# Optimization experiments

Hardware: AMD Instinct MI355X
Metric: run time of the kernel (lower is better)

## Reference

```python
import jax, jax.numpy as jnp
import numpy as np

N_NODES = 100000
N_EDGES = 1600000
D_IN = 128
D_H = 128
NEG_SLOPE = 0.2  # DGL GATConv default


def gat_layer(x, W, attn_l, attn_r, bias, src, dst, n_nodes):
    # x: [N, Din] -> h: [N, H]  (num_heads=1, head dim squeezed)
    h = x @ W
    el = jnp.einsum('nh,h->n', h, attn_l)  # [N]
    er = jnp.einsum('nh,h->n', h, attn_r)  # [N]
    e = jax.nn.leaky_relu(el[src] + er[dst], NEG_SLOPE)  # [E]
    # edge softmax over incoming edges of each dst node (numerically stable)
    m = jax.ops.segment_max(e, dst, num_segments=n_nodes)  # [N], -inf on zero-in-degree
    ex = jnp.exp(e - m[dst])  # [E]
    s = jax.ops.segment_sum(ex, dst, num_segments=n_nodes)  # [N]
    a = ex / s[dst]  # [E]
    out = jax.ops.segment_sum(a[:, None] * h[src], dst, num_segments=n_nodes)  # [N, H]
    return out + bias


def setup_inputs() -> dict:
    key = jax.random.key(0)
    ks = jax.random.split(key, 16)
    feat = jax.random.normal(ks[0], (N_NODES, D_IN), dtype=jnp.float32)
    src = jax.random.randint(ks[1], (N_EDGES,), 0, N_NODES, dtype=jnp.int32)
    dst = jax.random.randint(ks[2], (N_EDGES,), 0, N_NODES, dtype=jnp.int32)
    def xavier(k, shape):
        fan = sum(shape)
        return jax.random.normal(k, shape, dtype=jnp.float32) * jnp.sqrt(2.0 / fan)
    params = {}
    dims = [D_IN, D_H, D_H]
    for i in range(3):
        params[f'W{i+1}'] = xavier(ks[3 + 4 * i], (dims[i], D_H))
        params[f'al{i+1}'] = xavier(ks[4 + 4 * i], (D_H,))
        params[f'ar{i+1}'] = xavier(ks[5 + 4 * i], (D_H,))
        params[f'b{i+1}'] = jnp.zeros((D_H,), dtype=jnp.float32)
    return dict(feat=feat, src=src, dst=dst, **params)


def reference(feat, src, dst, W1, al1, ar1, b1, W2, al2, ar2, b2, W3, al3, ar3, b3):
    n = feat.shape[0]
    h = gat_layer(feat, W1, al1, ar1, b1, src, dst, n)
    h = gat_layer(h, W2, al2, ar2, b2, src, dst, n)
    h = gat_layer(h, W3, al3, ar3, b3, src, dst, n)
    return h  # [N, H] (head dim of size 1 squeezed)
```

## Files before the change

### kernel.cpp

```cpp
#include <hip/hip_runtime.h>

#define DH 128
#define NBMAX 1024
#define BCH 8192

typedef __attribute__((ext_vector_type(8))) short s16x8;
typedef __attribute__((ext_vector_type(4))) float f32x4;

__device__ __forceinline__ ushort f2bf(float x) {
  uint u = __builtin_bit_cast(uint, x);
  u = (u + 0x7FFF + ((u >> 16) & 1)) >> 16;
  return (ushort)u;
}
__device__ __forceinline__ float bfl2f(uint u) {
  return __builtin_bit_cast(float, u << 16);
}
__device__ __forceinline__ float bfh2f(uint u) {
  return __builtin_bit_cast(float, u & 0xFFFF0000u);
}


__global__ __launch_bounds__(256) void chist_kernel(const int* __restrict__ dst,
                                                    int* __restrict__ chist, int E, int NB) {
  __shared__ int h[NBMAX];
  int t = threadIdx.x;
  for (int i = t; i < NB; i += 256) h[i] = 0;
  __syncthreads();
  int base = blockIdx.x * BCH;
  int n = min(BCH, E - base);
  for (int i = t; i < n; i += 256) atomicAdd(&h[((uint)dst[base + i]) >> 7], 1);
  __syncthreads();
  for (int i = t; i < NB; i += 256)
    if (h[i]) atomicAdd(&chist[i * 16], h[i]);
}

__global__ __launch_bounds__(256) void cscan_kernel(const int* __restrict__ chist,
                                                    int* __restrict__ cbase, int* __restrict__ ccur,
                                                    int* __restrict__ rowptr, int N, int NB, int E) {
  __shared__ int lds[256];
  int t = threadIdx.x;
  int v[4], s = 0;
#pragma unroll
  for (int j = 0; j < 4; ++j) {
    int idx = t * 4 + j;
    v[j] = (idx < NB) ? chist[idx * 16] : 0;
    s += v[j];
  }
  lds[t] = s;
  __syncthreads();
  for (int off = 1; off < 256; off <<= 1) {
    int add = (t >= off) ? lds[t - off] : 0;
    __syncthreads();
    lds[t] += add;
    __syncthreads();
  }
  int run = t ? lds[t - 1] : 0;
#pragma unroll
  for (int j = 0; j < 4; ++j) {
    int idx = t * 4 + j;
    if (idx < NB) {
      cbase[idx] = run;
      ccur[idx * 16] = run;
    }
    run += v[j];
  }
  if (t == 255) cbase[NB] = lds[255];
  if (t == 0) rowptr[N] = E;
}

__global__ __launch_bounds__(256) void binscat_kernel(const int* __restrict__ src,
                                                      const int* __restrict__ dst,
                                                      int* __restrict__ ccur,
                                                      uint2* __restrict__ puv, int E, int NB) {
  __shared__ int h[NBMAX];
  __shared__ int gb[NBMAX];
  int t = threadIdx.x;
  int base = blockIdx.x * BCH;
  int n = min(BCH, E - base);
  for (int i = t; i < NB; i += 256) h[i] = 0;
  __syncthreads();
  for (int i = t; i < n; i += 256) atomicAdd(&h[((uint)dst[base + i]) >> 7], 1);
  __syncthreads();
  for (int i = t; i < NB; i += 256) {
    int c = h[i];
    gb[i] = c ? atomicAdd(&ccur[i * 16], c) : 0;
    h[i] = 0;
  }
  __syncthreads();
  for (int i = t; i < n; i += 256) {
    int d = dst[base + i];
    int b = ((uint)d) >> 7;
    int p = gb[b] + atomicAdd(&h[b], 1);
    puv[p] = make_uint2((uint)src[base + i], (uint)d);
  }
}

__global__ __launch_bounds__(256) void finesort_kernel(const uint2* __restrict__ puv,
                                                       const int* __restrict__ cbase,
                                                       int* __restrict__ rowptr,
                                                       int* __restrict__ ssrc, int N) {
  int b = blockIdx.x;
  int base = cbase[b];
  int cnt = cbase[b + 1] - base;
  __shared__ int ncnt[128], nincl[128], noff[128];
  int t = threadIdx.x;
  if (t < 128) ncnt[t] = 0;
  __syncthreads();
  for (int i = t; i < cnt; i += 256) atomicAdd(&ncnt[puv[base + i].y & 127], 1);
  __syncthreads();
  if (t < 128) nincl[t] = ncnt[t];
  __syncthreads();
  for (int off = 1; off < 128; off <<= 1) {
    int add = (t < 128 && t >= off) ? nincl[t - off] : 0;
    __syncthreads();
    if (t < 128) nincl[t] += add;
    __syncthreads();
  }
  if (t < 128) {
    noff[t] = nincl[t] - ncnt[t];
    int node = (b << 7) + t;
    if (node < N) rowptr[node] = base + noff[t];
    ncnt[t] = 0;
  }
  __syncthreads();
  for (int i = t; i < cnt; i += 256) {
    uint2 e = puv[base + i];
    int ln = e.y & 127;
    int p = base + noff[ln] + atomicAdd(&ncnt[ln], 1);
    ssrc[p] = (int)e.x;
  }
}

__global__ __launch_bounds__(256) void wt_kernel(const float* __restrict__ W,
                                                 ushort* __restrict__ Wtb) {
  int i = blockIdx.x * 256 + threadIdx.x;
  int col = i >> 7, k = i & 127;
  Wtb[(size_t)col * DH + k] = f2bf(W[(size_t)k * DH + col]);
}

template <bool XF32>
__global__ __launch_bounds__(256) void gemm_kernel(const void* __restrict__ xin,
                                                   const ushort* __restrict__ Wtb,
                                                   const float* __restrict__ al,
                                                   const float* __restrict__ ar,
                                                   ushort* __restrict__ hb,
                                                   float* __restrict__ el,
                                                   float* __restrict__ er, int M) {
  __shared__ ushort As[64 * DH];
  __shared__ ushort Bs[DH * DH];
  int t = threadIdx.x;
  int R0 = blockIdx.x * 64;

  for (int i = t; i < 2048; i += 256) {
    int col = i >> 4, kb = i & 15;
    s16x8 v = *(const s16x8*)(Wtb + (size_t)col * DH + kb * 8);
    *(s16x8*)(&Bs[col * DH + ((kb ^ (col & 15)) * 8)]) = v;
  }
  for (int i = t; i < 1024; i += 256) {
    int row = i >> 4, kb = i & 15;
    int gr = R0 + row;
    s16x8 v;
    if (gr < M) {
      if constexpr (XF32) {
        const float4* p = (const float4*)((const float*)xin + (size_t)gr * DH + kb * 8);
        float4 a = p[0], b = p[1];
        v[0] = (short)f2bf(a.x); v[1] = (short)f2bf(a.y);
        v[2] = (short)f2bf(a.z); v[3] = (short)f2bf(a.w);
        v[4] = (short)f2bf(b.x); v[5] = (short)f2bf(b.y);
        v[6] = (short)f2bf(b.z); v[7] = (short)f2bf(b.w);
      } else {
        v = *(const s16x8*)((const ushort*)xin + (size_t)gr * DH + kb * 8);
      }
    } else {
      v = (s16x8)0;
    }
    *(s16x8*)(&As[row * DH + ((kb ^ (row & 15)) * 8)]) = v;
  }
  __syncthreads();

  int w = t >> 6, lane = t & 63;
  int li = lane & 15, lq = lane >> 4;
  f32x4 acc[8] = {};
  int arow = w * 16 + li;
#pragma unroll
  for (int kc = 0; kc < 4; ++kc) {
    int kb = kc * 4 + lq;
    s16x8 af = *(const s16x8*)(&As[arow * DH + ((kb ^ (arow & 15)) * 8)]);
#pragma unroll
    for (int cf = 0; cf < 8; ++cf) {
      int bcol = cf * 16 + li;
      s16x8 bf = *(const s16x8*)(&Bs[bcol * DH + ((kb ^ (bcol & 15)) * 8)]);
      acc[cf] = __builtin_amdgcn_mfma_f32_16x16x32_bf16(af, bf, acc[cf], 0, 0, 0);
    }
  }

  int Rw = R0 + w * 16;
  float alv[8], arv[8];
#pragma unroll
  for (int cf = 0; cf < 8; ++cf) {
    alv[cf] = al[cf * 16 + li];
    arv[cf] = ar[cf * 16 + li];
  }
#pragma unroll
  for (int r = 0; r < 4; ++r) {
    float sl = 0.f, sr = 0.f;
#pragma unroll
    for (int cf = 0; cf < 8; ++cf) {
      sl += acc[cf][r] * alv[cf];
      sr += acc[cf][r] * arv[cf];
    }
#pragma unroll
    for (int off = 1; off <= 8; off <<= 1) {
      sl += __shfl_xor(sl, off);
      sr += __shfl_xor(sr, off);
    }
    int grow = Rw + lq * 4 + r;
    if (li == 0 && grow < M) {
      el[grow] = sl;
      er[grow] = sr;
    }
  }

  ushort* hl = &As[w * 16 * DH];
#pragma unroll
  for (int cf = 0; cf < 8; ++cf)
#pragma unroll
    for (int r = 0; r < 4; ++r) hl[(lq * 4 + r) * DH + cf * 16 + li] = f2bf(acc[cf][r]);
  __syncthreads();
#pragma unroll
  for (int p = 0; p < 4; ++p) {
    int row = lane >> 2;
    int blk = (lane & 3) + p * 4;
    s16x8 v = *(const s16x8*)(&hl[row * DH + blk * 8]);
    int grow = Rw + row;
    if (grow < M) *(s16x8*)(hb + (size_t)grow * DH + blk * 8) = v;
  }
}

template <int FINAL>
__global__ __launch_bounds__(256) void agg_kernel(const ushort* __restrict__ hb,
                                                  const float* __restrict__ el,
                                                  const float* __restrict__ er,
                                                  const int* __restrict__ rowptr,
                                                  const int* __restrict__ ssrc,
                                                  const float* __restrict__ bias,
                                                  void* __restrict__ outv, int M) {
  int wid = (blockIdx.x * blockDim.x + threadIdx.x) >> 6;
  int lane = threadIdx.x & 63;
  if (wid >= M) return;
  int begin = rowptr[wid], end = rowptr[wid + 1];
  float2 b2 = ((const float2*)bias)[lane];
  int deg = end - begin;
  float acc0 = 0.f, acc1 = 0.f;
  float inv = 0.f;

  if (deg > 0 && deg <= 64) {
    int e = begin + lane;
    int idx = (e < end) ? ssrc[e] : 0;
    float sc = -1e30f;
    if (e < end) {
      sc = el[idx] + er[wid];
      sc = sc > 0.f ? sc : 0.2f * sc;
    }
    float mx = sc;
#pragma unroll
    for (int off = 32; off; off >>= 1) mx = fmaxf(mx, __shfl_xor(mx, off));
    float wgt = (e < end) ? __expf(sc - mx) : 0.f;
    float ssum = wgt;
#pragma unroll
    for (int off = 32; off; off >>= 1) ssum += __shfl_xor(ssum, off);

    int j = 0;
    for (; j + 16 <= deg; j += 16) {
      uint u[16];
      float wg[16];
#pragma unroll
      for (int k = 0; k < 16; ++k) {
        int s = __shfl(idx, j + k);
        wg[k] = __shfl(wgt, j + k);
        u[k] = ((const uint*)(hb + (size_t)s * DH))[lane];
      }
#pragma unroll
      for (int k = 0; k < 16; ++k) {
        acc0 += wg[k] * bfl2f(u[k]);
        acc1 += wg[k] * bfh2f(u[k]);
      }
    }
    for (; j + 4 <= deg; j += 4) {
      uint u[4];
      float wg[4];
#pragma unroll
      for (int k = 0; k < 4; ++k) {
        int s = __shfl(idx, j + k);
        wg[k] = __shfl(wgt, j + k);
        u[k] = ((const uint*)(hb + (size_t)s * DH))[lane];
      }
#pragma unroll
      for (int k = 0; k < 4; ++k) {
        acc0 += wg[k] * bfl2f(u[k]);
        acc1 += wg[k] * bfh2f(u[k]);
      }
    }
    for (; j < deg; ++j) {
      int s = __shfl(idx, j);
      float wg = __shfl(wgt, j);
      uint u = ((const uint*)(hb + (size_t)s * DH))[lane];
      acc0 += wg * bfl2f(u);
      acc1 += wg * bfh2f(u);
    }
    inv = 1.f / ssum;
  } else if (deg > 64) {
    float er_d = er[wid];
    float mx = -1e30f;
    for (int e = begin + lane; e < end; e += 64) {
      float s = el[ssrc[e]] + er_d;
      s = s > 0.f ? s : 0.2f * s;
      mx = fmaxf(mx, s);
    }
#pragma unroll
    for (int off = 32; off; off >>= 1) mx = fmaxf(mx, __shfl_xor(mx, off));
    float ssum_l = 0.f;
    for (int base = begin; base < end; base += 64) {
      int n = min(64, end - base);
      int e = base + lane;
      int idx = 0;
      float wgt = 0.f;
      if (lane < n) {
        idx = ssrc[e];
        float sc = el[idx] + er_d;
        sc = sc > 0.f ? sc : 0.2f * sc;
        wgt = __expf(sc - mx);
      }
      ssum_l += wgt;
      int j = 0;
      for (; j + 4 <= n; j += 4) {
        uint u[4];
        float wg[4];
#pragma unroll
        for (int k = 0; k < 4; ++k) {
          int s = __shfl(idx, j + k);
          wg[k] = __shfl(wgt, j + k);
          u[k] = ((const uint*)(hb + (size_t)s * DH))[lane];
        }
#pragma unroll
        for (int k = 0; k < 4; ++k) {
          acc0 += wg[k] * bfl2f(u[k]);
          acc1 += wg[k] * bfh2f(u[k]);
        }
      }
      for (; j < n; ++j) {
        int s = __shfl(idx, j);
        float wg = __shfl(wgt, j);
        uint u = ((const uint*)(hb + (size_t)s * DH))[lane];
        acc0 += wg * bfl2f(u);
        acc1 += wg * bfh2f(u);
      }
    }
#pragma unroll
    for (int off = 32; off; off >>= 1) ssum_l += __shfl_xor(ssum_l, off);
    inv = 1.f / ssum_l;
  }
  float o0 = acc0 * inv + b2.x;
  float o1 = acc1 * inv + b2.y;
  if constexpr (FINAL) {
    ((float2*)((float*)outv + (size_t)wid * DH))[lane] = make_float2(o0, o1);
  } else {
    uint p = (uint)f2bf(o0) | ((uint)f2bf(o1) << 16);
    ((uint*)((ushort*)outv + (size_t)wid * DH))[lane] = p;
  }
}

extern "C" void kernel_launch(void* const* d_in, const int* in_sizes, int n_in,
                              void* d_out, int out_size, void* d_ws, size_t ws_size,
                              hipStream_t stream) {
  const float* feat = (const float*)d_in[0];
  const int* src = (const int*)d_in[1];
  const int* dst = (const int*)d_in[2];
  const int N = in_sizes[0] / DH;
  const int E = in_sizes[1];
  const int NB = (N + 127) >> 7;
  const float* W[3]  = {(const float*)d_in[3], (const float*)d_in[7],  (const float*)d_in[11]};
  const float* al[3] = {(const float*)d_in[4], (const float*)d_in[8],  (const float*)d_in[12]};
  const float* ar[3] = {(const float*)d_in[5], (const float*)d_in[9],  (const float*)d_in[13]};
  const float* bi[3] = {(const float*)d_in[6], (const float*)d_in[10], (const float*)d_in[14]};

  char* ws = (char*)d_ws;
  size_t off = 0;
  auto alloc = [&](size_t bytes) {
    void* p = ws + off;
    off = (off + bytes + 255) & ~(size_t)255;
    return p;
  };
  ushort* hb   = (ushort*)alloc((size_t)N * DH * sizeof(ushort));
  ushort* xb   = (ushort*)alloc((size_t)N * DH * sizeof(ushort));
  float* el    = (float*)alloc((size_t)N * sizeof(float));
  float* er    = (float*)alloc((size_t)N * sizeof(float));
  int* rowptr  = (int*)alloc((size_t)(N + 1) * sizeof(int));
  int* ssrc    = (int*)alloc((size_t)E * sizeof(int));
  ushort* Wtb  = (ushort*)alloc((size_t)DH * DH * sizeof(ushort));
  int* chist   = (int*)alloc((size_t)NBMAX * 16 * sizeof(int));
  int* cbase   = (int*)alloc((size_t)(NBMAX + 1) * sizeof(int));
  int* ccur    = (int*)alloc((size_t)NBMAX * 16 * sizeof(int));
  uint2* puv   = (uint2*)hb;

  hipMemsetAsync(chist, 0, (size_t)NBMAX * 16 * sizeof(int), stream);
  int ebl = (E + BCH - 1) / BCH;
  chist_kernel<<<ebl, 256, 0, stream>>>(dst, chist, E, NB);
  cscan_kernel<<<1, 256, 0, stream>>>(chist, cbase, ccur, rowptr, N, NB, E);
  binscat_kernel<<<ebl, 256, 0, stream>>>(src, dst, ccur, puv, E, NB);
  finesort_kernel<<<NB, 256, 0, stream>>>(puv, cbase, rowptr, ssrc, N);

  for (int l = 0; l < 3; ++l) {
    wt_kernel<<<64, 256, 0, stream>>>(W[l], Wtb);
    if (l == 0)
      gemm_kernel<true><<<(N + 63) / 64, 256, 0, stream>>>(feat, Wtb, al[l], ar[l], hb, el, er, N);
    else
      gemm_kernel<false><<<(N + 63) / 64, 256, 0, stream>>>(xb, Wtb, al[l], ar[l], hb, el, er, N);
    if (l < 2)
      agg_kernel<0><<<(N + 3) / 4, 256, 0, stream>>>(hb, el, er, rowptr, ssrc, bi[l], xb, N);
    else
      agg_kernel<1><<<(N + 3) / 4, 256, 0, stream>>>(hb, el, er, rowptr, ssrc, bi[l], d_out, N);
  }
}
```

Before: 344.8 us.

## Pack sort keys into 32 bits and gather 16-byte rows per quarter-wave in aggregation

The bin scatter now stores each edge as one 32-bit word, with the low 7 bits of dst in the top bits and src in the low 25 bits, instead of a uint2. This halves the scatter and fine-sort traffic. In the low-degree aggregation path, each quarter-wave now loads a full 256-byte row as 16-byte vectors, so four edges are gathered per instruction. Partial sums are then reduced across quarters with shuffles and written by 16 lanes using vector stores. The change adds cross-lane reduction cost and assumes node ids fit in 25 bits, and it drops the unrolling in the high-degree path.

```diff
diff --git a/kernel.cpp b/kernel.cpp
--- a/kernel.cpp
+++ b/kernel.cpp
@@ -71,7 +71,7 @@
 __global__ __launch_bounds__(256) void binscat_kernel(const int* __restrict__ src,
                                                       const int* __restrict__ dst,
                                                       int* __restrict__ ccur,
-                                                      uint2* __restrict__ puv, int E, int NB) {
+                                                      uint* __restrict__ puv, int E, int NB) {
   __shared__ int h[NBMAX];
   __shared__ int gb[NBMAX];
   int t = threadIdx.x;
@@ -88,14 +88,14 @@
   }
   __syncthreads();
   for (int i = t; i < n; i += 256) {
-    int d = dst[base + i];
-    int b = ((uint)d) >> 7;
+    uint d = (uint)dst[base + i];
+    int b = d >> 7;
     int p = gb[b] + atomicAdd(&h[b], 1);
-    puv[p] = make_uint2((uint)src[base + i], (uint)d);
-  }
-}
-
-__global__ __launch_bounds__(256) void finesort_kernel(const uint2* __restrict__ puv,
+    puv[p] = ((d & 127u) << 25) | (uint)src[base + i];
+  }
+}
+
+__global__ __launch_bounds__(256) void finesort_kernel(const uint* __restrict__ puv,
                                                        const int* __restrict__ cbase,
                                                        int* __restrict__ rowptr,
                                                        int* __restrict__ ssrc, int N) {
@@ -106,7 +106,7 @@
   int t = threadIdx.x;
   if (t < 128) ncnt[t] = 0;
   __syncthreads();
-  for (int i = t; i < cnt; i += 256) atomicAdd(&ncnt[puv[base + i].y & 127], 1);
+  for (int i = t; i < cnt; i += 256) atomicAdd(&ncnt[puv[base + i] >> 25], 1);
   __syncthreads();
   if (t < 128) nincl[t] = ncnt[t];
   __syncthreads();
@@ -124,10 +124,10 @@
   }
   __syncthreads();
   for (int i = t; i < cnt; i += 256) {
-    uint2 e = puv[base + i];
-    int ln = e.y & 127;
+    uint e = puv[base + i];
+    int ln = e >> 25;
     int p = base + noff[ln] + atomicAdd(&ncnt[ln], 1);
-    ssrc[p] = (int)e.x;
+    ssrc[p] = (int)(e & 0x1FFFFFFu);
   }
 }
 
@@ -249,67 +249,9 @@
   int lane = threadIdx.x & 63;
   if (wid >= M) return;
   int begin = rowptr[wid], end = rowptr[wid + 1];
-  float2 b2 = ((const float2*)bias)[lane];
   int deg = end - begin;
-  float acc0 = 0.f, acc1 = 0.f;
-  float inv = 0.f;
-
-  if (deg > 0 && deg <= 64) {
-    int e = begin + lane;
-    int idx = (e < end) ? ssrc[e] : 0;
-    float sc = -1e30f;
-    if (e < end) {
-      sc = el[idx] + er[wid];
-      sc = sc > 0.f ? sc : 0.2f * sc;
-    }
-    float mx = sc;
-#pragma unroll
-    for (int off = 32; off; off >>= 1) mx = fmaxf(mx, __shfl_xor(mx, off));
-    float wgt = (e < end) ? __expf(sc - mx) : 0.f;
-    float ssum = wgt;
-#pragma unroll
-    for (int off = 32; off; off >>= 1) ssum += __shfl_xor(ssum, off);
-
-    int j = 0;
-    for (; j + 16 <= deg; j += 16) {
-      uint u[16];
-      float wg[16];
-#pragma unroll
-      for (int k = 0; k < 16; ++k) {
-        int s = __shfl(idx, j + k);
-        wg[k] = __shfl(wgt, j + k);
-        u[k] = ((const uint*)(hb + (size_t)s * DH))[lane];
-      }
-#pragma unroll
-      for (int k = 0; k < 16; ++k) {
-        acc0 += wg[k] * bfl2f(u[k]);
-        acc1 += wg[k] * bfh2f(u[k]);
-      }
-    }
-    for (; j + 4 <= deg; j += 4) {
-      uint u[4];
-      float wg[4];
-#pragma unroll
-      for (int k = 0; k < 4; ++k) {
-        int s = __shfl(idx, j + k);
-        wg[k] = __shfl(wgt, j + k);
-        u[k] = ((const uint*)(hb + (size_t)s * DH))[lane];
-      }
-#pragma unroll
-      for (int k = 0; k < 4; ++k) {
-        acc0 += wg[k] * bfl2f(u[k]);
-        acc1 += wg[k] * bfh2f(u[k]);
-      }
-    }
-    for (; j < deg; ++j) {
-      int s = __shfl(idx, j);
-      float wg = __shfl(wgt, j);
-      uint u = ((const uint*)(hb + (size_t)s * DH))[lane];
-      acc0 += wg * bfl2f(u);
-      acc1 += wg * bfh2f(u);
-    }
-    inv = 1.f / ssum;
-  } else if (deg > 64) {
+
+  if (deg > 64) {
     float er_d = er[wid];
     float mx = -1e30f;
     for (int e = begin + lane; e < end; e += 64) {
@@ -319,7 +261,7 @@
     }
 #pragma unroll
     for (int off = 32; off; off >>= 1) mx = fmaxf(mx, __shfl_xor(mx, off));
-    float ssum_l = 0.f;
+    float acc0 = 0.f, acc1 = 0.f, ssum_l = 0.f;
     for (int base = begin; base < end; base += 64) {
       int n = min(64, end - base);
       int e = base + lane;
@@ -332,23 +274,7 @@
         wgt = __expf(sc - mx);
       }
       ssum_l += wgt;
-      int j = 0;
-      for (; j + 4 <= n; j += 4) {
-        uint u[4];
-        float wg[4];
-#pragma unroll
-        for (int k = 0; k < 4; ++k) {
-          int s = __shfl(idx, j + k);
-          wg[k] = __shfl(wgt, j + k);
-          u[k] = ((const uint*)(hb + (size_t)s * DH))[lane];
-        }
-#pragma unroll
-        for (int k = 0; k < 4; ++k) {
-          acc0 += wg[k] * bfl2f(u[k]);
-          acc1 += wg[k] * bfh2f(u[k]);
-        }
-      }
-      for (; j < n; ++j) {
+      for (int j = 0; j < n; ++j) {
         int s = __shfl(idx, j);
         float wg = __shfl(wgt, j);
         uint u = ((const uint*)(hb + (size_t)s * DH))[lane];
@@ -358,15 +284,84 @@
     }
 #pragma unroll
     for (int off = 32; off; off >>= 1) ssum_l += __shfl_xor(ssum_l, off);
-    inv = 1.f / ssum_l;
-  }
-  float o0 = acc0 * inv + b2.x;
-  float o1 = acc1 * inv + b2.y;
-  if constexpr (FINAL) {
-    ((float2*)((float*)outv + (size_t)wid * DH))[lane] = make_float2(o0, o1);
-  } else {
-    uint p = (uint)f2bf(o0) | ((uint)f2bf(o1) << 16);
-    ((uint*)((ushort*)outv + (size_t)wid * DH))[lane] = p;
+    float inv = 1.f / ssum_l;
+    float2 b2 = ((const float2*)bias)[lane];
+    float o0 = acc0 * inv + b2.x;
+    float o1 = acc1 * inv + b2.y;
+    if constexpr (FINAL) {
+      ((float2*)((float*)outv + (size_t)wid * DH))[lane] = make_float2(o0, o1);
+    } else {
+      uint p = (uint)f2bf(o0) | ((uint)f2bf(o1) << 16);
+      ((uint*)((ushort*)outv + (size_t)wid * DH))[lane] = p;
+    }
+    return;
+  }
+
+  float acc[8] = {};
+  float inv = 0.f;
+  if (deg > 0) {
+    int e = begin + lane;
+    int idx = (e < end) ? ssrc[e] : 0;
+    float sc = -1e30f;
+    if (e < end) {
+      sc = el[idx] + er[wid];
+      sc = sc > 0.f ? sc : 0.2f * sc;
+    }
+    float mx = sc;
+#pragma unroll
+    for (int off = 32; off; off >>= 1) mx = fmaxf(mx, __shfl_xor(mx, off));
+    float wgt = (e < end) ? __expf(sc - mx) : 0.f;
+    float ssum = wgt;
+#pragma unroll
+    for (int off = 32; off; off >>= 1) ssum += __shfl_xor(ssum, off);
+    inv = 1.f / ssum;
+
+    int q = lane >> 4, cl = lane & 15;
+    const uint4* hb4 = (const uint4*)hb;
+    for (int j = 0; j < deg; j += 16) {
+      uint4 u[4];
+      float wq[4];
+#pragma unroll
+      for (int k = 0; k < 4; ++k) {
+        int ej = j + k * 4 + q;
+        int s = __shfl(idx, ej);
+        wq[k] = __shfl(wgt, ej);
+        u[k] = hb4[(size_t)s * 16 + cl];
+      }
+#pragma unroll
+      for (int k = 0; k < 4; ++k) {
+        acc[0] += wq[k] * bfl2f(u[k].x); acc[1] += wq[k] * bfh2f(u[k].x);
+        acc[2] += wq[k] * bfl2f(u[k].y); acc[3] += wq[k] * bfh2f(u[k].y);
+        acc[4] += wq[k] * bfl2f(u[k].z); acc[5] += wq[k] * bfh2f(u[k].z);
+        acc[6] += wq[k] * bfl2f(u[k].w); acc[7] += wq[k] * bfh2f(u[k].w);
+      }
+    }
+#pragma unroll
+    for (int i = 0; i < 8; ++i) {
+      acc[i] += __shfl_xor(acc[i], 16);
+      acc[i] += __shfl_xor(acc[i], 32);
+    }
+  }
+  if (lane < 16) {
+    float4 b0 = ((const float4*)bias)[lane * 2];
+    float4 b1 = ((const float4*)bias)[lane * 2 + 1];
+    float o[8];
+    o[0] = acc[0] * inv + b0.x; o[1] = acc[1] * inv + b0.y;
+    o[2] = acc[2] * inv + b0.z; o[3] = acc[3] * inv + b0.w;
+    o[4] = acc[4] * inv + b1.x; o[5] = acc[5] * inv + b1.y;
+    o[6] = acc[6] * inv + b1.z; o[7] = acc[7] * inv + b1.w;
+    if constexpr (FINAL) {
+      float* op = (float*)outv + (size_t)wid * DH + lane * 8;
+      *(float4*)op = make_float4(o[0], o[1], o[2], o[3]);
+      *(float4*)(op + 4) = make_float4(o[4], o[5], o[6], o[7]);
+    } else {
+      uint4 p;
+      p.x = (uint)f2bf(o[0]) | ((uint)f2bf(o[1]) << 16);
+      p.y = (uint)f2bf(o[2]) | ((uint)f2bf(o[3]) << 16);
+      p.z = (uint)f2bf(o[4]) | ((uint)f2bf(o[5]) << 16);
+      p.w = (uint)f2bf(o[6]) | ((uint)f2bf(o[7]) << 16);
+      ((uint4*)((ushort*)outv + (size_t)wid * DH))[lane] = p;
+    }
   }
 }
 
@@ -401,7 +396,7 @@
   int* chist   = (int*)alloc((size_t)NBMAX * 16 * sizeof(int));
   int* cbase   = (int*)alloc((size_t)(NBMAX + 1) * sizeof(int));
   int* ccur    = (int*)alloc((size_t)NBMAX * 16 * sizeof(int));
-  uint2* puv   = (uint2*)hb;
+  uint* puv    = (uint*)hb;
 
   hipMemsetAsync(chist, 0, (size_t)NBMAX * 16 * sizeof(int), stream);
   int ebl = (E + BCH - 1) / BCH;
```

After: 341.0 us. No clear change (-1.1%).
